# Performance work log

Measured on AMD Instinct MI355X. Metric: run time of the kernel, lower is better.

The kernel has to match this reference:

```python
import jax, jax.numpy as jnp
import numpy as np

B, S, C, V = 8, 256, 256, 64

def setup_inputs() -> dict:
    key = jax.random.key(0)
    ks = jax.random.split(key, 11)
    bound = 1.0 / np.sqrt(C)
    u = lambda k, shape: jax.random.uniform(k, shape, jnp.float32, -bound, bound)
    return {
        "ctx": jax.random.normal(ks[0], (B, S, C), jnp.float32),
        "W": u(ks[1], (C, C, V)),
        "bias": u(ks[2], (V,)),
        "lin1_w": u(ks[3], (V, C)), "lin1_b": u(ks[4], (V,)),
        "lin2_w": u(ks[5], (V, C)), "lin2_b": u(ks[6], (V,)),
        "linmul_w": u(ks[7], (V, C)), "linmul_b": u(ks[8], (V,)),
        "lindiff_w": u(ks[9], (V, C)), "lindiff_b": u(ks[10], (V,)),
    }

def reference(ctx, W, bias, lin1_w, lin1_b, lin2_w, lin2_b,
              linmul_w, linmul_b, lindiff_w, lindiff_b):
    # bilinear: out[b,s,z,k] = sum_ij ctx[b,s,i] * ctx[b,z,j] * W[i,j,k]
    tmp = jnp.einsum('bsi,ijk->bsjk', ctx, W)          # (B,S,C,V)
    out = jnp.einsum('bsjk,bzj->bszk', tmp, ctx)       # (B,S,S,V)
    out = out + bias
    out1 = ctx @ lin1_w.T + lin1_b                     # (B,S,V)
    out2 = ctx @ lin2_w.T + lin2_b                     # (B,S,V)
    # mul[b,s,z] = ctx[b,z] * ctx[b,s]; diff[b,s,z] = ctx[b,z] - ctx[b,s]
    mul = ctx[:, None, :, :] * ctx[:, :, None, :]      # (B,S,S,C)
    diff = ctx[:, None, :, :] - ctx[:, :, None, :]     # (B,S,S,C)
    outmul = mul @ linmul_w.T + linmul_b               # (B,S,S,V)
    outdiff = diff @ lindiff_w.T + lindiff_b           # (B,S,S,V)
    return jnp.tanh(out + out1[:, None, :, :] + out2[:, :, None, :] + outmul + outdiff)
```

## Files before the change

kernel.cpp:

```cpp
#include <hip/hip_runtime.h>


typedef __attribute__((ext_vector_type(8))) _Float16 half8;
typedef __attribute__((ext_vector_type(4))) _Float16 half4v;
typedef __attribute__((ext_vector_type(4))) float f32x4;

__device__ __forceinline__ void async16(const void* g, void* l) {
  __builtin_amdgcn_global_load_lds(
      (__attribute__((address_space(1))) void*)g,
      (__attribute__((address_space(3))) void*)l, 16, 0, 0);
}

__global__ __launch_bounds__(256) void prep_ctx(const float* __restrict__ ctx,
                                                _Float16* __restrict__ ch) {
  int idx = (blockIdx.x * 256 + threadIdx.x) * 4;
  float4 v = *(const float4*)(ctx + idx);
  half4v o;
  o[0] = (_Float16)v.x; o[1] = (_Float16)v.y;
  o[2] = (_Float16)v.z; o[3] = (_Float16)v.w;
  *(half4v*)(ch + idx) = o;
}

__global__ __launch_bounds__(256) void prep_wt(const float* __restrict__ W,
                                               const float* __restrict__ lmw,
                                               _Float16* __restrict__ wt) {
  __shared__ _Float16 T[256 * 68];
  const int t = threadIdx.x;
  const int j = blockIdx.x;
#pragma unroll
  for (int p = 0; p < 16; ++p) {
    int i = p * 16 + (t >> 4);
    int c = t & 15;
    float4 v = *(const float4*)&W[(size_t)i * 16384 + j * 64 + c * 4];
    if (i == j) {
      v.x += lmw[(c * 4 + 0) * 256 + j];
      v.y += lmw[(c * 4 + 1) * 256 + j];
      v.z += lmw[(c * 4 + 2) * 256 + j];
      v.w += lmw[(c * 4 + 3) * 256 + j];
    }
    half4v o;
    o[0] = (_Float16)v.x; o[1] = (_Float16)v.y;
    o[2] = (_Float16)v.z; o[3] = (_Float16)v.w;
    *(half4v*)&T[i * 68 + c * 4] = o;
  }
  __syncthreads();
  const int k = t >> 2, i0 = (t & 3) * 64;
  _Float16* dst = wt + ((size_t)(k * 256 + j)) * 256 + i0;
#pragma unroll
  for (int u = 0; u < 64; u += 8) {
    half8 o;
#pragma unroll
    for (int e = 0; e < 8; ++e) o[e] = T[(i0 + u + e) * 68 + k];
    *(half8*)(dst + u) = o;
  }
}

__global__ __launch_bounds__(256) void prep_rt(
    const float* __restrict__ ctx, const float* __restrict__ bias,
    const float* __restrict__ l1w, const float* __restrict__ l1b,
    const float* __restrict__ l2w, const float* __restrict__ l2b,
    const float* __restrict__ lmb, const float* __restrict__ ldw,
    const float* __restrict__ ldb, float* __restrict__ rbuf,
    float* __restrict__ tbuf) {
  __shared__ float Cs[4 * 256];
  const int t = threadIdx.x;
  const int row0 = blockIdx.x * 4;
  ((float4*)Cs)[t] = ((const float4*)(ctx + (size_t)row0 * 256))[t];
  __syncthreads();
  const int k = t & 63, lr = t >> 6;
  const float* l1r = l1w + k * 256;
  const float* l2r = l2w + k * 256;
  const float* ldr = ldw + k * 256;
  float a1 = 0.f, a2 = 0.f;
  for (int c = 0; c < 256; c += 4) {
    float4 w1 = *(const float4*)(l1r + c);
    float4 w2 = *(const float4*)(l2r + c);
    float4 wd = *(const float4*)(ldr + c);
    float4 cv = *(const float4*)(&Cs[lr * 256 + c]);
    a1 += cv.x * (w1.x + wd.x) + cv.y * (w1.y + wd.y) +
          cv.z * (w1.z + wd.z) + cv.w * (w1.w + wd.w);
    a2 += cv.x * (w2.x - wd.x) + cv.y * (w2.y - wd.y) +
          cv.z * (w2.z - wd.z) + cv.w * (w2.w - wd.w);
  }
  int row = row0 + lr;
  rbuf[row * 64 + k] = a1 + l1b[k];
  tbuf[row * 64 + k] = a2 + l2b[k] + bias[k] + lmb[k] + ldb[k];
}

__global__ __launch_bounds__(256) void gemm1(const _Float16* __restrict__ ch,
                                             const _Float16* __restrict__ wt,
                                             _Float16* __restrict__ tmp) {
  __shared__ _Float16 pool[4 * 64 * 72];
  _Float16* As = pool;
  _Float16* Bs = pool + 4096;
  const int t = threadIdx.x;
  const int lane = t & 63, wave = t >> 6;
  const int m0 = blockIdx.y * 128, n0 = blockIdx.x * 128;
  const int wm = (wave & 1) * 64, wn = (wave >> 1) * 64;
  const int r = lane & 15, q = lane >> 4;
  f32x4 acc[4][4] = {};
  const _Float16* gA = ch + (size_t)(m0 + (t >> 2)) * 256 + (t & 3) * 8;
  const _Float16* gB = wt + (size_t)(n0 + (t >> 2)) * 256 + (t & 3) * 8;
  for (int k0 = 0; k0 < 256; k0 += 32) {
    async16(gA + k0, &As[t * 8]);
    async16(gA + 64 * 256 + k0, &As[2048 + t * 8]);
    async16(gB + k0, &Bs[t * 8]);
    async16(gB + 64 * 256 + k0, &Bs[2048 + t * 8]);
    __syncthreads();
    half8 a[4], b[4];
#pragma unroll
    for (int mi = 0; mi < 4; ++mi)
      a[mi] = *(const half8*)&As[(wm + mi * 16 + r) * 32 + q * 8];
#pragma unroll
    for (int ni = 0; ni < 4; ++ni)
      b[ni] = *(const half8*)&Bs[(wn + ni * 16 + r) * 32 + q * 8];
#pragma unroll
    for (int ni = 0; ni < 4; ++ni)
#pragma unroll
      for (int mi = 0; mi < 4; ++mi)
        acc[ni][mi] = __builtin_amdgcn_mfma_f32_16x16x32_f16(b[ni], a[mi],
                                                             acc[ni][mi], 0, 0, 0);
    __syncthreads();
  }
  _Float16* Sw = pool + wave * 4608;
#pragma unroll
  for (int ni = 0; ni < 4; ++ni)
#pragma unroll
    for (int mi = 0; mi < 4; ++mi) {
      half4v h;
#pragma unroll
      for (int e = 0; e < 4; ++e) h[e] = (_Float16)acc[ni][mi][e];
      *(half4v*)&Sw[(mi * 16 + r) * 72 + ni * 16 + q * 4] = h;
    }
  __syncthreads();
  const int g2 = lane >> 3, c2 = lane & 7;
  _Float16* dst = tmp + (size_t)(m0 + wm) * 16384 + (n0 + wn);
#pragma unroll
  for (int u = 0; u < 8; ++u) {
    int row = u * 8 + g2;
    half8 vv = *(const half8*)&Sw[row * 72 + c2 * 8];
    *(half8*)(dst + (size_t)row * 16384 + c2 * 8) = vv;
  }
}

__global__ __launch_bounds__(256) void gemm2(const _Float16* __restrict__ ch,
                                             const _Float16* __restrict__ tmp,
                                             const float* __restrict__ rbuf,
                                             const float* __restrict__ tbuf,
                                             float* __restrict__ out) {
  __shared__ _Float16 As[256 * 32];
  __shared__ _Float16 Bs[64 * 32];
  __shared__ float Ts[64];
  const int t = threadIdx.x;
  const int lane = t & 63, wave = t >> 6;
  const int bs = blockIdx.x;
  const int b = bs >> 8;
  const int r = lane & 15, q = lane >> 4;
  const _Float16* ctxb = ch + (size_t)b * 65536;
  const _Float16* tm = tmp + (size_t)bs * 16384;
  if (t < 64) Ts[t] = tbuf[bs * 64 + t];
  f32x4 acc[4][4] = {};
  for (int j0 = 0; j0 < 256; j0 += 32) {
#pragma unroll
    for (int p = 0; p < 4; ++p)
      async16(ctxb + (size_t)(p * 64 + (t >> 2)) * 256 + j0 + (t & 3) * 8,
              &As[p * 2048 + t * 8]);
    async16(tm + (size_t)(t >> 2) * 256 + j0 + (t & 3) * 8, &Bs[t * 8]);
    __syncthreads();
    half8 a[4], bf[4];
#pragma unroll
    for (int zi = 0; zi < 4; ++zi)
      a[zi] = *(const half8*)&As[(wave * 64 + zi * 16 + r) * 32 + q * 8];
#pragma unroll
    for (int ki = 0; ki < 4; ++ki)
      bf[ki] = *(const half8*)&Bs[(ki * 16 + r) * 32 + q * 8];
#pragma unroll
    for (int ki = 0; ki < 4; ++ki)
#pragma unroll
      for (int zi = 0; zi < 4; ++zi)
        acc[ki][zi] = __builtin_amdgcn_mfma_f32_16x16x32_f16(bf[ki], a[zi],
                                                             acc[ki][zi], 0, 0, 0);
    __syncthreads();
  }
  const float* rb = rbuf + (size_t)b * 16384;
#pragma unroll
  for (int ki = 0; ki < 4; ++ki)
#pragma unroll
    for (int zi = 0; zi < 4; ++zi) {
      int z = wave * 64 + zi * 16 + r;
      int k = ki * 16 + q * 4;
      f32x4 rv = *(const f32x4*)&rb[z * 64 + k];
      f32x4 tv = *(const f32x4*)&Ts[k];
      f32x4 o;
#pragma unroll
      for (int e = 0; e < 4; ++e) {
        float x = acc[ki][zi][e] + rv[e] + tv[e];
        float ax = fabsf(x);
        float ev = __expf(-2.0f * ax);
        float y = (1.0f - ev) / (1.0f + ev);
        o[e] = copysignf(y, x);
      }
      *(f32x4*)&out[((size_t)bs * 256 + z) * 64 + k] = o;
    }
}

extern "C" void kernel_launch(void* const* d_in, const int* in_sizes, int n_in,
                              void* d_out, int out_size, void* d_ws, size_t ws_size,
                              hipStream_t stream) {
  const float* ctx  = (const float*)d_in[0];
  const float* W    = (const float*)d_in[1];
  const float* bias = (const float*)d_in[2];
  const float* l1w  = (const float*)d_in[3];
  const float* l1b  = (const float*)d_in[4];
  const float* l2w  = (const float*)d_in[5];
  const float* l2b  = (const float*)d_in[6];
  const float* lmw  = (const float*)d_in[7];
  const float* lmb  = (const float*)d_in[8];
  const float* ldw  = (const float*)d_in[9];
  const float* ldb  = (const float*)d_in[10];
  float* out = (float*)d_out;

  char* ws = (char*)d_ws;
  _Float16* ch  = (_Float16*)ws;
  _Float16* wt  = (_Float16*)(ws + (1u << 20));
  _Float16* tmp = (_Float16*)(ws + (9u << 20));
  float* rbuf = (float*)(ws + (73u << 20));
  float* tbuf = rbuf + 2048 * 64;

  prep_ctx<<<512, 256, 0, stream>>>(ctx, ch);
  prep_wt<<<256, 256, 0, stream>>>(W, lmw, wt);
  prep_rt<<<512, 256, 0, stream>>>(ctx, bias, l1w, l1b, l2w, l2b, lmb, ldw, ldb,
                                   rbuf, tbuf);
  gemm1<<<dim3(128, 16), 256, 0, stream>>>(ch, wt, tmp);
  gemm2<<<2048, 256, 0, stream>>>(ch, tmp, rbuf, tbuf, out);
}
```

Before: 280.8 us.

## Widen GEMM K-tiles to 64 with XOR-swizzled LDS, remap blocks for XCD locality

Both GEMM kernels now stage 64-wide K slices per iteration, which halves the number of barrier pairs. The LDS layout uses an XOR swizzle on 16-byte column groups to avoid bank conflicts on the half8 fragment reads. Block indices are remapped so that consecutive blocks on the same XCD share A/tmp data, aiming for better L2 reuse. prep_rt now computes 16 rows per block and reuses the combined weight vectors across 4 rows per thread. The cost is larger LDS per block, which may reduce occupancy.

```diff
diff --git a/kernel.cpp b/kernel.cpp
--- a/kernel.cpp
+++ b/kernel.cpp
@@ -62,29 +62,42 @@
     const float* __restrict__ lmb, const float* __restrict__ ldw,
     const float* __restrict__ ldb, float* __restrict__ rbuf,
     float* __restrict__ tbuf) {
-  __shared__ float Cs[4 * 256];
-  const int t = threadIdx.x;
-  const int row0 = blockIdx.x * 4;
-  ((float4*)Cs)[t] = ((const float4*)(ctx + (size_t)row0 * 256))[t];
+  __shared__ float Cs[16 * 256];
+  const int t = threadIdx.x;
+  const int row0 = blockIdx.x * 16;
+#pragma unroll
+  for (int p = 0; p < 4; ++p)
+    ((float4*)Cs)[p * 256 + t] =
+        ((const float4*)(ctx + (size_t)row0 * 256))[p * 256 + t];
   __syncthreads();
   const int k = t & 63, lr = t >> 6;
   const float* l1r = l1w + k * 256;
   const float* l2r = l2w + k * 256;
   const float* ldr = ldw + k * 256;
-  float a1 = 0.f, a2 = 0.f;
+  float a1[4] = {0.f, 0.f, 0.f, 0.f};
+  float a2[4] = {0.f, 0.f, 0.f, 0.f};
   for (int c = 0; c < 256; c += 4) {
     float4 w1 = *(const float4*)(l1r + c);
     float4 w2 = *(const float4*)(l2r + c);
     float4 wd = *(const float4*)(ldr + c);
-    float4 cv = *(const float4*)(&Cs[lr * 256 + c]);
-    a1 += cv.x * (w1.x + wd.x) + cv.y * (w1.y + wd.y) +
-          cv.z * (w1.z + wd.z) + cv.w * (w1.w + wd.w);
-    a2 += cv.x * (w2.x - wd.x) + cv.y * (w2.y - wd.y) +
-          cv.z * (w2.z - wd.z) + cv.w * (w2.w - wd.w);
-  }
-  int row = row0 + lr;
-  rbuf[row * 64 + k] = a1 + l1b[k];
-  tbuf[row * 64 + k] = a2 + l2b[k] + bias[k] + lmb[k] + ldb[k];
+    float4 s1, s2;
+    s1.x = w1.x + wd.x; s1.y = w1.y + wd.y; s1.z = w1.z + wd.z; s1.w = w1.w + wd.w;
+    s2.x = w2.x - wd.x; s2.y = w2.y - wd.y; s2.z = w2.z - wd.z; s2.w = w2.w - wd.w;
+#pragma unroll
+    for (int u = 0; u < 4; ++u) {
+      float4 cv = *(const float4*)(&Cs[(lr * 4 + u) * 256 + c]);
+      a1[u] += cv.x * s1.x + cv.y * s1.y + cv.z * s1.z + cv.w * s1.w;
+      a2[u] += cv.x * s2.x + cv.y * s2.y + cv.z * s2.z + cv.w * s2.w;
+    }
+  }
+  float tb = l2b[k] + bias[k] + lmb[k] + ldb[k];
+  float rb = l1b[k];
+#pragma unroll
+  for (int u = 0; u < 4; ++u) {
+    int row = row0 + lr * 4 + u;
+    rbuf[row * 64 + k] = a1[u] + rb;
+    tbuf[row * 64 + k] = a2[u] + tb;
+  }
 }
 
 __global__ __launch_bounds__(256) void gemm1(const _Float16* __restrict__ ch,
@@ -92,34 +105,43 @@
                                              _Float16* __restrict__ tmp) {
   __shared__ _Float16 pool[4 * 64 * 72];
   _Float16* As = pool;
-  _Float16* Bs = pool + 4096;
+  _Float16* Bs = pool + 8192;
   const int t = threadIdx.x;
   const int lane = t & 63, wave = t >> 6;
-  const int m0 = blockIdx.y * 128, n0 = blockIdx.x * 128;
+  const int d = blockIdx.x + blockIdx.y * 128;
+  const int w = (d & 7) * 256 + (d >> 3);
+  const int m0 = (w & 15) * 128, n0 = (w >> 4) * 128;
   const int wm = (wave & 1) * 64, wn = (wave >> 1) * 64;
   const int r = lane & 15, q = lane >> 4;
+  const int sr = r & 7;
   f32x4 acc[4][4] = {};
-  const _Float16* gA = ch + (size_t)(m0 + (t >> 2)) * 256 + (t & 3) * 8;
-  const _Float16* gB = wt + (size_t)(n0 + (t >> 2)) * 256 + (t & 3) * 8;
-  for (int k0 = 0; k0 < 256; k0 += 32) {
-    async16(gA + k0, &As[t * 8]);
-    async16(gA + 64 * 256 + k0, &As[2048 + t * 8]);
-    async16(gB + k0, &Bs[t * 8]);
-    async16(gB + 64 * 256 + k0, &Bs[2048 + t * 8]);
-    __syncthreads();
-    half8 a[4], b[4];
-#pragma unroll
-    for (int mi = 0; mi < 4; ++mi)
-      a[mi] = *(const half8*)&As[(wm + mi * 16 + r) * 32 + q * 8];
-#pragma unroll
-    for (int ni = 0; ni < 4; ++ni)
-      b[ni] = *(const half8*)&Bs[(wn + ni * 16 + r) * 32 + q * 8];
-#pragma unroll
-    for (int ni = 0; ni < 4; ++ni)
+  const int cg = (t & 7) ^ ((t >> 3) & 7);
+  const _Float16* gA = ch + (size_t)(m0 + (t >> 3)) * 256 + cg * 8;
+  const _Float16* gB = wt + (size_t)(n0 + (t >> 3)) * 256 + cg * 8;
+  for (int k0 = 0; k0 < 256; k0 += 64) {
+#pragma unroll
+    for (int p = 0; p < 4; ++p) {
+      async16(gA + p * 32 * 256 + k0, &As[p * 2048 + t * 8]);
+      async16(gB + p * 32 * 256 + k0, &Bs[p * 2048 + t * 8]);
+    }
+    __syncthreads();
+#pragma unroll
+    for (int kk = 0; kk < 2; ++kk) {
+      const int ca = ((kk * 4 + q) ^ sr) * 8;
+      half8 a[4], b[4];
 #pragma unroll
       for (int mi = 0; mi < 4; ++mi)
-        acc[ni][mi] = __builtin_amdgcn_mfma_f32_16x16x32_f16(b[ni], a[mi],
-                                                             acc[ni][mi], 0, 0, 0);
+        a[mi] = *(const half8*)&As[(wm + mi * 16 + r) * 64 + ca];
+#pragma unroll
+      for (int ni = 0; ni < 4; ++ni)
+        b[ni] = *(const half8*)&Bs[(wn + ni * 16 + r) * 64 + ca];
+#pragma unroll
+      for (int ni = 0; ni < 4; ++ni)
+#pragma unroll
+        for (int mi = 0; mi < 4; ++mi)
+          acc[ni][mi] = __builtin_amdgcn_mfma_f32_16x16x32_f16(
+              b[ni], a[mi], acc[ni][mi], 0, 0, 0);
+    }
     __syncthreads();
   }
   _Float16* Sw = pool + wave * 4608;
@@ -148,38 +170,48 @@
                                              const float* __restrict__ rbuf,
                                              const float* __restrict__ tbuf,
                                              float* __restrict__ out) {
-  __shared__ _Float16 As[256 * 32];
-  __shared__ _Float16 Bs[64 * 32];
+  __shared__ _Float16 As[256 * 64];
+  __shared__ _Float16 Bs[64 * 64];
   __shared__ float Ts[64];
   const int t = threadIdx.x;
   const int lane = t & 63, wave = t >> 6;
-  const int bs = blockIdx.x;
+  const int d = blockIdx.x;
+  const int bs = (d & 7) * 256 + (d >> 3);
   const int b = bs >> 8;
   const int r = lane & 15, q = lane >> 4;
+  const int sr = r & 7;
   const _Float16* ctxb = ch + (size_t)b * 65536;
   const _Float16* tm = tmp + (size_t)bs * 16384;
   if (t < 64) Ts[t] = tbuf[bs * 64 + t];
   f32x4 acc[4][4] = {};
-  for (int j0 = 0; j0 < 256; j0 += 32) {
-#pragma unroll
-    for (int p = 0; p < 4; ++p)
-      async16(ctxb + (size_t)(p * 64 + (t >> 2)) * 256 + j0 + (t & 3) * 8,
-              &As[p * 2048 + t * 8]);
-    async16(tm + (size_t)(t >> 2) * 256 + j0 + (t & 3) * 8, &Bs[t * 8]);
-    __syncthreads();
-    half8 a[4], bf[4];
-#pragma unroll
-    for (int zi = 0; zi < 4; ++zi)
-      a[zi] = *(const half8*)&As[(wave * 64 + zi * 16 + r) * 32 + q * 8];
-#pragma unroll
-    for (int ki = 0; ki < 4; ++ki)
-      bf[ki] = *(const half8*)&Bs[(ki * 16 + r) * 32 + q * 8];
-#pragma unroll
-    for (int ki = 0; ki < 4; ++ki)
+  const int cg = (t & 7) ^ ((t >> 3) & 7);
+  const _Float16* gA = ctxb + (size_t)(t >> 3) * 256 + cg * 8;
+  const _Float16* gB = tm + (size_t)(t >> 3) * 256 + cg * 8;
+  for (int j0 = 0; j0 < 256; j0 += 64) {
+#pragma unroll
+    for (int p = 0; p < 8; ++p)
+      async16(gA + p * 32 * 256 + j0, &As[p * 2048 + t * 8]);
+#pragma unroll
+    for (int p = 0; p < 2; ++p)
+      async16(gB + p * 32 * 256 + j0, &Bs[p * 2048 + t * 8]);
+    __syncthreads();
+#pragma unroll
+    for (int kk = 0; kk < 2; ++kk) {
+      const int ca = ((kk * 4 + q) ^ sr) * 8;
+      half8 a[4], bf[4];
 #pragma unroll
       for (int zi = 0; zi < 4; ++zi)
-        acc[ki][zi] = __builtin_amdgcn_mfma_f32_16x16x32_f16(bf[ki], a[zi],
-                                                             acc[ki][zi], 0, 0, 0);
+        a[zi] = *(const half8*)&As[(wave * 64 + zi * 16 + r) * 64 + ca];
+#pragma unroll
+      for (int ki = 0; ki < 4; ++ki)
+        bf[ki] = *(const half8*)&Bs[(ki * 16 + r) * 64 + ca];
+#pragma unroll
+      for (int ki = 0; ki < 4; ++ki)
+#pragma unroll
+        for (int zi = 0; zi < 4; ++zi)
+          acc[ki][zi] = __builtin_amdgcn_mfma_f32_16x16x32_f16(
+              bf[ki], a[zi], acc[ki][zi], 0, 0, 0);
+    }
     __syncthreads();
   }
   const float* rb = rbuf + (size_t)b * 16384;
@@ -229,7 +261,7 @@
 
   prep_ctx<<<512, 256, 0, stream>>>(ctx, ch);
   prep_wt<<<256, 256, 0, stream>>>(W, lmw, wt);
-  prep_rt<<<512, 256, 0, stream>>>(ctx, bias, l1w, l1b, l2w, l2b, lmb, ldw, ldb,
+  prep_rt<<<128, 256, 0, stream>>>(ctx, bias, l1w, l1b, l2w, l2b, lmb, ldw, ldb,
                                    rbuf, tbuf);
   gemm1<<<dim3(128, 16), 256, 0, stream>>>(ch, wt, tmp);
   gemm2<<<2048, 256, 0, stream>>>(ch, tmp, rbuf, tbuf, out);
```

Measured after the change: 247.9 us. 1.13x faster.
